# Kernel tuning notes

Measured on AMD Instinct MI355X. Metric: run time of the kernel, lower is better.

Reference implementation:

```python
import jax, jax.numpy as jnp
import numpy as np

B, S, D, H = 4, 2048, 1024, 16
DH = D // H


def setup_inputs() -> dict:
    key = jax.random.key(0)
    ks = jax.random.split(key, 7)
    return {
        "Q": jax.random.normal(ks[0], (B, S, D), dtype=jnp.float32),
        "K": jax.random.normal(ks[1], (B, S, D), dtype=jnp.float32),
        "V": jax.random.normal(ks[2], (B, S, D), dtype=jnp.float32),
        "q_proj": jax.random.normal(ks[3], (D, D), dtype=jnp.float32),
        "k_proj": jax.random.normal(ks[4], (D, D), dtype=jnp.float32),
        "v_proj": jax.random.normal(ks[5], (D, D), dtype=jnp.float32),
        "output_proj": jax.random.normal(ks[6], (D, D), dtype=jnp.float32),
        "casual": 1,
    }


def reference(Q, K, V, q_proj, k_proj, v_proj, output_proj, casual):
    # projections: einsum('... a b, ... s b -> ... s a') == x @ W.T
    q = jnp.einsum('bsd,ad->bsa', Q, q_proj)
    k = jnp.einsum('bsd,ad->bsa', K, k_proj)
    v = jnp.einsum('bsd,ad->bsa', V, v_proj)
    # split heads: [B, S, H, DH]
    q = q.reshape(B, S, H, DH)
    k = k.reshape(B, S, H, DH)
    v = v.reshape(B, S, H, DH)
    # scores [B, H, Sq, Sk]
    scores = jnp.einsum('bqhd,bkhd->bhqk', q, k) / np.sqrt(DH).astype(np.float32)
    # causal mask: 0 on lower triangle, -inf above
    causal_mask = jnp.where(
        jnp.tril(jnp.ones((S, S), dtype=bool)), 0.0, -jnp.inf
    ).astype(scores.dtype)
    scores = scores + causal_mask
    attn = jax.nn.softmax(scores, axis=-1)
    # weighted values -> [B, Sq, H, DH] -> [B, Sq, D]
    out = jnp.einsum('bhqk,bkhd->bqhd', attn, v).reshape(B, S, D)
    # output projection: einsum('... a b, ... b -> ... a') == x @ W.T
    return jnp.einsum('bsd,ad->bsa', out, output_proj)
```

## Files before the change

### kernel.cpp

```cpp
#include <hip/hip_runtime.h>


typedef __attribute__((ext_vector_type(8))) _Float16 half8;
typedef __attribute__((ext_vector_type(4))) float f32x4;

#define DEVI static __device__ __forceinline__

static constexpr int cB = 4, cS = 2048, cD = 1024, cH = 16, cDH = 64;
static constexpr int cM = cB * cS;

DEVI unsigned short h2b(_Float16 h) { union { _Float16 f; unsigned short u; } x; x.f = h; return x.u; }

DEVI void async16(const void* g, void* l) {
#if defined(__HIP_DEVICE_COMPILE__)
  __builtin_amdgcn_global_load_lds((const __attribute__((address_space(1))) unsigned int*)g,
                                   (__attribute__((address_space(3))) unsigned int*)l, 16, 0, 0);
#endif
}

__global__ void split4_kernel(const float* __restrict__ Wq, const float* __restrict__ Wk,
                              const float* __restrict__ Wv, const float* __restrict__ Wo,
                              unsigned short* __restrict__ Wqh, unsigned short* __restrict__ Wql,
                              unsigned short* __restrict__ Wkh, unsigned short* __restrict__ Wkl,
                              unsigned short* __restrict__ Wvh, unsigned short* __restrict__ Woh) {
  const int w = blockIdx.x >> 10, blk = blockIdx.x & 1023;
  const float* in = (w == 0) ? Wq : (w == 1) ? Wk : (w == 2) ? Wv : Wo;
  unsigned short* hi = (w == 0) ? Wqh : (w == 1) ? Wkh : (w == 2) ? Wvh : Woh;
  unsigned short* lo = (w == 0) ? Wql : (w == 1) ? Wkl : nullptr;
  int i = (blk * 256 + (int)threadIdx.x) * 4;
  float4 v = *(const float4*)(in + i);
  _Float16 h0 = (_Float16)v.x, h1 = (_Float16)v.y, h2 = (_Float16)v.z, h3 = (_Float16)v.w;
  unsigned short th[4] = {h2b(h0), h2b(h1), h2b(h2), h2b(h3)};
  *(uint2*)(hi + i) = *(const uint2*)th;
  if (lo != nullptr) {
    unsigned short tl[4] = {h2b((_Float16)(v.x - (float)h0)), h2b((_Float16)(v.y - (float)h1)),
                            h2b((_Float16)(v.z - (float)h2)), h2b((_Float16)(v.w - (float)h3))};
    *(uint2*)(lo + i) = *(const uint2*)tl;
  }
}

__global__ void split_act_kernel(const float* __restrict__ Q, const float* __restrict__ K,
                                 unsigned short* __restrict__ Qh, unsigned short* __restrict__ Ql,
                                 unsigned short* __restrict__ Kh, unsigned short* __restrict__ Kl) {
  const int t = blockIdx.x >> 13;
  const int blk = blockIdx.x & 8191;
  const float* in = t ? K : Q;
  unsigned short* hi = t ? Kh : Qh;
  unsigned short* lo = t ? Kl : Ql;
  int i = (blk * 256 + (int)threadIdx.x) * 4;
  float4 v = *(const float4*)(in + i);
  _Float16 h0 = (_Float16)v.x, h1 = (_Float16)v.y, h2 = (_Float16)v.z, h3 = (_Float16)v.w;
  unsigned short th[4] = {h2b(h0), h2b(h1), h2b(h2), h2b(h3)};
  *(uint2*)(hi + i) = *(const uint2*)th;
  unsigned short tl[4] = {h2b((_Float16)(v.x - (float)h0)), h2b((_Float16)(v.y - (float)h1)),
                          h2b((_Float16)(v.z - (float)h2)), h2b((_Float16)(v.w - (float)h3))};
  *(uint2*)(lo + i) = *(const uint2*)tl;
}

__global__ __launch_bounds__(256, 2) void proj_qk(
    const unsigned short* __restrict__ Qh, const unsigned short* __restrict__ Ql,
    const unsigned short* __restrict__ Kh, const unsigned short* __restrict__ Kl,
    const unsigned short* __restrict__ Wqh, const unsigned short* __restrict__ Wql,
    const unsigned short* __restrict__ Wkh, const unsigned short* __restrict__ Wkl,
    unsigned short* __restrict__ qph, unsigned short* __restrict__ qpl,
    unsigned short* __restrict__ kph, unsigned short* __restrict__ kpl) {
  constexpr int N = cD, K = cD;
  __shared__ unsigned short sAh[2][128 * 32];
  __shared__ unsigned short sAl[2][128 * 32];
  __shared__ unsigned short sBh[2][128 * 32];
  __shared__ unsigned short sBl[2][128 * 32];

  const int wid = ((int)blockIdx.x & 7) * 128 + ((int)blockIdx.x >> 3);
  const int job = wid >> 9;
  const int bid = wid & 511;
  const unsigned short* Ah_g = job ? Kh : Qh;
  const unsigned short* Al_g = job ? Kl : Ql;
  const unsigned short* Bh = job ? Wkh : Wqh;
  const unsigned short* Bl = job ? Wkl : Wql;
  unsigned short* C0 = job ? kph : qph;
  unsigned short* C1 = job ? kpl : qpl;

  const int tid = threadIdx.x, lane = tid & 63, wave = tid >> 6;
  const int wm = wave >> 1, wn = wave & 1;
  const int bm = bid >> 3, bn = bid & 7;
  const long r0 = (long)bm * 128, c0 = (long)bn * 128;
  const int quad = lane >> 4, cl = lane & 15;
  const int lrow16 = lane >> 2, lg4 = lane & 3;

  f32x4 acc[4][4];
#pragma unroll
  for (int mt = 0; mt < 4; ++mt)
#pragma unroll
    for (int nt = 0; nt < 4; ++nt) acc[mt][nt] = f32x4{0.f, 0.f, 0.f, 0.f};

  auto stage = [&](int k0, int buf) {
#pragma unroll
    for (int c = 0; c < 2; ++c) {
      int cc = wave * 2 + c;
      int r = cc * 16 + lrow16;
      int sw = (lg4 ^ ((lrow16 >> 1) & 3)) * 8;
      long ga = (r0 + r) * (long)K + k0 + sw;
      long gb = (c0 + r) * (long)K + k0 + sw;
      async16(Ah_g + ga, &sAh[buf][cc * 512]);
      async16(Al_g + ga, &sAl[buf][cc * 512]);
      async16(Bh + gb, &sBh[buf][cc * 512]);
      async16(Bl + gb, &sBl[buf][cc * 512]);
    }
  };

  auto compute = [&](int buf) {
    half8 ah[4], al[4], bh8[4], bl8[4];
#pragma unroll
    for (int mt = 0; mt < 4; ++mt) {
      int r = wm * 64 + mt * 16 + cl;
      int s = quad ^ ((r >> 1) & 3);
      ah[mt] = *(const half8*)(&sAh[buf][r * 32 + s * 8]);
      al[mt] = *(const half8*)(&sAl[buf][r * 32 + s * 8]);
    }
#pragma unroll
    for (int nt = 0; nt < 4; ++nt) {
      int r = wn * 64 + nt * 16 + cl;
      int s = quad ^ ((r >> 1) & 3);
      bh8[nt] = *(const half8*)(&sBh[buf][r * 32 + s * 8]);
      bl8[nt] = *(const half8*)(&sBl[buf][r * 32 + s * 8]);
    }
#pragma unroll
    for (int mt = 0; mt < 4; ++mt)
#pragma unroll
      for (int nt = 0; nt < 4; ++nt) {
        acc[mt][nt] = __builtin_amdgcn_mfma_f32_16x16x32_f16(ah[mt], bh8[nt], acc[mt][nt], 0, 0, 0);
        acc[mt][nt] = __builtin_amdgcn_mfma_f32_16x16x32_f16(ah[mt], bl8[nt], acc[mt][nt], 0, 0, 0);
        acc[mt][nt] = __builtin_amdgcn_mfma_f32_16x16x32_f16(al[mt], bh8[nt], acc[mt][nt], 0, 0, 0);
      }
  };

  stage(0, 0);
  __syncthreads();
  int cur = 0;
  for (int k0 = 32; k0 < K; k0 += 32) {
    stage(k0, cur ^ 1);
    compute(cur);
    __syncthreads();
    cur ^= 1;
  }
  compute(cur);

#pragma unroll
  for (int mt = 0; mt < 4; ++mt)
#pragma unroll
    for (int nt = 0; nt < 4; ++nt)
#pragma unroll
      for (int i = 0; i < 4; ++i) {
        long row = r0 + wm * 64 + mt * 16 + quad * 4 + i;
        long col = c0 + wn * 64 + nt * 16 + cl;
        float v = acc[mt][nt][i];
        _Float16 hh = (_Float16)v;
        C0[row * N + col] = h2b(hh);
        C1[row * N + col] = h2b((_Float16)(v - (float)hh));
      }
}

__global__ __launch_bounds__(256, 3) void proj_v(const float* __restrict__ Va,
                                                 const unsigned short* __restrict__ Wvh,
                                                 unsigned short* __restrict__ vp) {
  constexpr int N = cD, K = cD;
  __shared__ float sA32[2][128 * 32];
  __shared__ unsigned short sBh[2][128 * 32];

  const int wid = ((int)blockIdx.x & 7) * 64 + ((int)blockIdx.x >> 3);
  const int bm = wid >> 3, bn = wid & 7;
  const long r0 = (long)bm * 128, c0 = (long)bn * 128;

  const int tid = threadIdx.x, lane = tid & 63, wave = tid >> 6;
  const int wm = wave >> 1, wn = wave & 1;
  const int quad = lane >> 4, cl = lane & 15;
  const int lrow8 = lane >> 3, lg8 = lane & 7;
  const int lrow16 = lane >> 2, lg4 = lane & 3;

  f32x4 acc[4][4];
#pragma unroll
  for (int mt = 0; mt < 4; ++mt)
#pragma unroll
    for (int nt = 0; nt < 4; ++nt) acc[mt][nt] = f32x4{0.f, 0.f, 0.f, 0.f};

  auto stage = [&](int k0, int buf) {
#pragma unroll
    for (int c = 0; c < 4; ++c) {
      int cc = wave * 4 + c;
      int r = cc * 8 + lrow8;
      const float* g = Va + (r0 + r) * (long)K + k0 + ((lg8 ^ lrow8) * 4);
      async16(g, &sA32[buf][cc * 256]);
    }
#pragma unroll
    for (int c = 0; c < 2; ++c) {
      int cc = wave * 2 + c;
      int r = cc * 16 + lrow16;
      long gb = (c0 + r) * (long)K + k0 + ((lg4 ^ ((lrow16 >> 1) & 3)) * 8);
      async16(Wvh + gb, &sBh[buf][cc * 512]);
    }
  };

  auto compute = [&](int buf) {
    half8 ah[4], bh8[4];
#pragma unroll
    for (int mt = 0; mt < 4; ++mt) {
      int r = wm * 64 + mt * 16 + cl;
      int s0 = (quad * 2 + 0) ^ (r & 7), s1 = (quad * 2 + 1) ^ (r & 7);
      float fa[8];
      *(float4*)(fa) = *(const float4*)(&sA32[buf][r * 32 + s0 * 4]);
      *(float4*)(fa + 4) = *(const float4*)(&sA32[buf][r * 32 + s1 * 4]);
#pragma unroll
      for (int j = 0; j < 8; ++j) ah[mt][j] = (_Float16)fa[j];
    }
#pragma unroll
    for (int nt = 0; nt < 4; ++nt) {
      int r = wn * 64 + nt * 16 + cl;
      int s = quad ^ ((r >> 1) & 3);
      bh8[nt] = *(const half8*)(&sBh[buf][r * 32 + s * 8]);
    }
#pragma unroll
    for (int mt = 0; mt < 4; ++mt)
#pragma unroll
      for (int nt = 0; nt < 4; ++nt)
        acc[mt][nt] = __builtin_amdgcn_mfma_f32_16x16x32_f16(ah[mt], bh8[nt], acc[mt][nt], 0, 0, 0);
  };

  stage(0, 0);
  __syncthreads();
  int cur = 0;
  for (int k0 = 32; k0 < K; k0 += 32) {
    stage(k0, cur ^ 1);
    compute(cur);
    __syncthreads();
    cur ^= 1;
  }
  compute(cur);

#pragma unroll
  for (int mt = 0; mt < 4; ++mt)
#pragma unroll
    for (int nt = 0; nt < 4; ++nt)
#pragma unroll
      for (int i = 0; i < 4; ++i) {
        long row = r0 + wm * 64 + mt * 16 + quad * 4 + i;
        long col = c0 + wn * 64 + nt * 16 + cl;
        vp[row * N + col] = h2b((_Float16)acc[mt][nt][i]);
      }
}

__global__ __launch_bounds__(256, 3) void gemm_out(const unsigned short* __restrict__ A16p,
                                                   const unsigned short* __restrict__ Bh,
                                                   float* __restrict__ C0, int M, int N, int K) {
  __shared__ unsigned short sA16[2][128 * 32];
  __shared__ unsigned short sB16[2][128 * 32];

  const int tid = threadIdx.x, lane = tid & 63, wave = tid >> 6;
  const int wm = wave >> 1, wn = wave & 1;
  const int nb = N >> 7;
  const int wid = ((int)blockIdx.x & 7) * 64 + ((int)blockIdx.x >> 3);
  const int bm = wid / nb, bn = wid % nb;
  const long r0 = (long)bm * 128, c0 = (long)bn * 128;
  const int quad = lane >> 4, cl = lane & 15;
  const int lrow16 = lane >> 2, lg4 = lane & 3;

  f32x4 acc[4][4];
#pragma unroll
  for (int mt = 0; mt < 4; ++mt)
#pragma unroll
    for (int nt = 0; nt < 4; ++nt) acc[mt][nt] = f32x4{0.f, 0.f, 0.f, 0.f};

  auto stage = [&](int k0, int buf) {
#pragma unroll
    for (int c = 0; c < 2; ++c) {
      int cc = wave * 2 + c;
      int r = cc * 16 + lrow16;
      int sw = (lg4 ^ ((lrow16 >> 1) & 3)) * 8;
      async16(A16p + (r0 + r) * (long)K + k0 + sw, &sA16[buf][cc * 512]);
      async16(Bh + (c0 + r) * (long)K + k0 + sw, &sB16[buf][cc * 512]);
    }
  };

  auto compute = [&](int buf) {
    half8 ah[4], bh8[4];
#pragma unroll
    for (int mt = 0; mt < 4; ++mt) {
      int r = wm * 64 + mt * 16 + cl;
      int s = quad ^ ((r >> 1) & 3);
      ah[mt] = *(const half8*)(&sA16[buf][r * 32 + s * 8]);
    }
#pragma unroll
    for (int nt = 0; nt < 4; ++nt) {
      int r = wn * 64 + nt * 16 + cl;
      int s = quad ^ ((r >> 1) & 3);
      bh8[nt] = *(const half8*)(&sB16[buf][r * 32 + s * 8]);
    }
#pragma unroll
    for (int mt = 0; mt < 4; ++mt)
#pragma unroll
      for (int nt = 0; nt < 4; ++nt)
        acc[mt][nt] = __builtin_amdgcn_mfma_f32_16x16x32_f16(ah[mt], bh8[nt], acc[mt][nt], 0, 0, 0);
  };

  stage(0, 0);
  __syncthreads();
  int cur = 0;
  for (int k0 = 32; k0 < K; k0 += 32) {
    stage(k0, cur ^ 1);
    compute(cur);
    __syncthreads();
    cur ^= 1;
  }
  compute(cur);

#pragma unroll
  for (int mt = 0; mt < 4; ++mt)
#pragma unroll
    for (int nt = 0; nt < 4; ++nt)
#pragma unroll
      for (int i = 0; i < 4; ++i) {
        long row = r0 + wm * 64 + mt * 16 + quad * 4 + i;
        long col = c0 + wn * 64 + nt * 16 + cl;
        C0[row * N + col] = acc[mt][nt][i];
      }
}

__global__ __launch_bounds__(256, 3) void flash_kernel(
    const unsigned short* __restrict__ qh_g, const unsigned short* __restrict__ ql_g,
    const unsigned short* __restrict__ kh_g, const unsigned short* __restrict__ kl_g,
    const unsigned short* __restrict__ vp_g, unsigned short* __restrict__ out) {
  __shared__ unsigned short sKh[64 * 64];
  __shared__ unsigned short sKl[64 * 64];
  __shared__ unsigned int sVtU[64 * 34];
  __shared__ unsigned short sP[4][32 * 40];

  const int tid = threadIdx.x, lane = tid & 63, wave = tid >> 6;
  const int quad = lane >> 4, cl = lane & 15;
  const int bh = blockIdx.x & 63;
  const int qt = 15 - (blockIdx.x >> 6);
  const int h = bh & 15;
  const int b = bh >> 4;
  const long rowbase = (long)b * cS;
  const int q0 = qt * 128;
  const int lrow8 = lane >> 3, lg8 = lane & 7;

  half8 qh[2][2], ql[2][2];
  const _Float16 s8 = (_Float16)0.125f;
#pragma unroll
  for (int ks = 0; ks < 2; ++ks)
#pragma unroll
    for (int mt = 0; mt < 2; ++mt) {
      long r = rowbase + q0 + wave * 32 + mt * 16 + cl;
      long off = r * cD + h * 64 + ks * 32 + quad * 8;
      qh[ks][mt] = *(const half8*)(qh_g + off) * s8;
      ql[ks][mt] = *(const half8*)(ql_g + off) * s8;
    }

  f32x4 O[2][5];
  float mrow[2][4];
#pragma unroll
  for (int mt = 0; mt < 2; ++mt) {
#pragma unroll
    for (int dt = 0; dt < 5; ++dt) O[mt][dt] = f32x4{0.f, 0.f, 0.f, 0.f};
#pragma unroll
    for (int i = 0; i < 4; ++i) mrow[mt][i] = -1e30f;
  }

  half8 vone;
#pragma unroll
  for (int j = 0; j < 8; ++j) vone[j] = (cl == 0) ? (_Float16)1.0f : (_Float16)0.0f;

  auto tile = [&](int ki, bool MASK) {
    __syncthreads();
#pragma unroll
    for (int c = 0; c < 2; ++c) {
      int cc = wave * 2 + c;
      int r = cc * 8 + lrow8;
      long g = (rowbase + ki * 64 + r) * (long)cD + h * 64 + ((lg8 ^ lrow8) * 8);
      async16(kh_g + g, sKh + cc * 512);
      async16(kl_g + g, sKl + cc * 512);
    }
    {
      int r2 = tid & 31, dc = (tid >> 5) * 8;
      const unsigned short* gv = vp_g + (rowbase + ki * 64 + 2 * r2) * (long)cD + h * 64 + dc;
      unsigned short a[8], bb[8];
      *(uint4*)a = *(const uint4*)gv;
      *(uint4*)bb = *(const uint4*)(gv + cD);
#pragma unroll
      for (int j = 0; j < 8; ++j)
        sVtU[(dc + j) * 34 + r2] = (unsigned int)a[j] | ((unsigned int)bb[j] << 16);
    }
    __syncthreads();

    f32x4 sacc[2][4];
#pragma unroll
    for (int mt = 0; mt < 2; ++mt)
#pragma unroll
      for (int nt = 0; nt < 4; ++nt) sacc[mt][nt] = f32x4{0.f, 0.f, 0.f, 0.f};
#pragma unroll
    for (int ks = 0; ks < 2; ++ks) {
      half8 kh8[4], kl8[4];
#pragma unroll
      for (int nt = 0; nt < 4; ++nt) {
        int r = nt * 16 + cl;
        int off = r * 64 + (((ks * 4 + quad) ^ (r & 7)) * 8);
        kh8[nt] = *(const half8*)(sKh + off);
        kl8[nt] = *(const half8*)(sKl + off);
      }
#pragma unroll
      for (int mt = 0; mt < 2; ++mt)
#pragma unroll
        for (int nt = 0; nt < 4; ++nt) {
          sacc[mt][nt] = __builtin_amdgcn_mfma_f32_16x16x32_f16(qh[ks][mt], kh8[nt], sacc[mt][nt], 0, 0, 0);
          sacc[mt][nt] = __builtin_amdgcn_mfma_f32_16x16x32_f16(qh[ks][mt], kl8[nt], sacc[mt][nt], 0, 0, 0);
          sacc[mt][nt] = __builtin_amdgcn_mfma_f32_16x16x32_f16(ql[ks][mt], kh8[nt], sacc[mt][nt], 0, 0, 0);
        }
    }
    if (MASK) {
#pragma unroll
      for (int mt = 0; mt < 2; ++mt)
#pragma unroll
        for (int nt = 0; nt < 4; ++nt)
#pragma unroll
          for (int i = 0; i < 4; ++i) {
            int rg = q0 + wave * 32 + mt * 16 + quad * 4 + i;
            int cg = ki * 64 + nt * 16 + cl;
            if (cg > rg) sacc[mt][nt][i] = -1e30f;
          }
    }
    float mnew[2][4];
    bool ch = false;
#pragma unroll
    for (int mt = 0; mt < 2; ++mt)
#pragma unroll
      for (int i = 0; i < 4; ++i) {
        float mx = fmaxf(fmaxf(sacc[mt][0][i], sacc[mt][1][i]),
                         fmaxf(sacc[mt][2][i], sacc[mt][3][i]));
#pragma unroll
        for (int d = 1; d < 16; d <<= 1) mx = fmaxf(mx, __shfl_xor(mx, d));
        ch |= (mx > mrow[mt][i]);
        mnew[mt][i] = fmaxf(mrow[mt][i], mx);
      }
    if (__ballot(ch)) {
#pragma unroll
      for (int mt = 0; mt < 2; ++mt)
#pragma unroll
        for (int i = 0; i < 4; ++i) {
          float a = __expf(mrow[mt][i] - mnew[mt][i]);
#pragma unroll
          for (int dt = 0; dt < 5; ++dt) O[mt][dt][i] *= a;
        }
    }
#pragma unroll
    for (int mt = 0; mt < 2; ++mt)
#pragma unroll
      for (int i = 0; i < 4; ++i) mrow[mt][i] = mnew[mt][i];

    unsigned short* sPw = sP[wave];
#pragma unroll
    for (int kc = 0; kc < 2; ++kc) {
#pragma unroll
      for (int mt = 0; mt < 2; ++mt)
#pragma unroll
        for (int ntl = 0; ntl < 2; ++ntl) {
          int nt = kc * 2 + ntl;
#pragma unroll
          for (int i = 0; i < 4; ++i) {
            float p = __expf(sacc[mt][nt][i] - mrow[mt][i]);
            sPw[(mt * 16 + quad * 4 + i) * 40 + ntl * 16 + cl] = h2b((_Float16)p);
          }
        }
      half8 pa[2], vb[4];
#pragma unroll
      for (int mt = 0; mt < 2; ++mt)
        pa[mt] = *(const half8*)(sPw + (mt * 16 + cl) * 40 + quad * 8);
#pragma unroll
      for (int dt = 0; dt < 4; ++dt) {
        int base = (dt * 16 + cl) * 34 + kc * 16 + quad * 4;
        union { uint4 u; half8 hh; } cvt;
        uint2 p0 = *(const uint2*)(sVtU + base);
        uint2 p1 = *(const uint2*)(sVtU + base + 2);
        cvt.u = uint4{p0.x, p0.y, p1.x, p1.y};
        vb[dt] = cvt.hh;
      }
#pragma unroll
      for (int mt = 0; mt < 2; ++mt) {
#pragma unroll
        for (int dt = 0; dt < 4; ++dt)
          O[mt][dt] = __builtin_amdgcn_mfma_f32_16x16x32_f16(pa[mt], vb[dt], O[mt][dt], 0, 0, 0);
        O[mt][4] = __builtin_amdgcn_mfma_f32_16x16x32_f16(pa[mt], vone, O[mt][4], 0, 0, 0);
      }
    }
  };

  const int full = 2 * qt;
  for (int ki = 0; ki < full; ++ki) tile(ki, false);
  tile(full, true);
  tile(full + 1, true);

  float lv[2][4];
#pragma unroll
  for (int mt = 0; mt < 2; ++mt)
#pragma unroll
    for (int i = 0; i < 4; ++i) lv[mt][i] = __shfl(O[mt][4][i], (lane & 48));
#pragma unroll
  for (int mt = 0; mt < 2; ++mt)
#pragma unroll
    for (int dt = 0; dt < 4; ++dt)
#pragma unroll
      for (int i = 0; i < 4; ++i) {
        long r = rowbase + q0 + wave * 32 + mt * 16 + quad * 4 + i;
        out[r * cD + h * 64 + dt * 16 + cl] = h2b((_Float16)(O[mt][dt][i] / lv[mt][i]));
      }
}

extern "C" void kernel_launch(void* const* d_in, const int* in_sizes, int n_in,
                              void* d_out, int out_size, void* d_ws, size_t ws_size,
                              hipStream_t stream) {
  const float* Q = (const float*)d_in[0];
  const float* K = (const float*)d_in[1];
  const float* V = (const float*)d_in[2];
  const float* Wq = (const float*)d_in[3];
  const float* Wk = (const float*)d_in[4];
  const float* Wv = (const float*)d_in[5];
  const float* Wo = (const float*)d_in[6];

  unsigned short* ws = (unsigned short*)d_ws;
  const size_t WD = (size_t)cD * cD;
  const size_t WM = (size_t)cM * cD;
  unsigned short* Wqh = ws;
  unsigned short* Wql = Wqh + WD;
  unsigned short* Wkh = Wql + WD;
  unsigned short* Wkl = Wkh + WD;
  unsigned short* Wvh = Wkl + WD;
  unsigned short* Woh = Wvh + WD;
  unsigned short* R1 = Woh + WD;
  unsigned short* R2 = R1 + WM;
  unsigned short* qph = R2 + WM;
  unsigned short* qpl = qph + WM;
  unsigned short* kph = qpl + WM;
  unsigned short* kpl = kph + WM;

  unsigned short* Qh = (unsigned short*)d_out;
  unsigned short* Ql = Qh + WM;
  unsigned short* Kh = R1;
  unsigned short* Kl = R2;
  unsigned short* vp = R1;
  unsigned short* attnb = R2;

  split4_kernel<<<4096, 256, 0, stream>>>(Wq, Wk, Wv, Wo, Wqh, Wql, Wkh, Wkl, Wvh, Woh);
  split_act_kernel<<<16384, 256, 0, stream>>>(Q, K, Qh, Ql, Kh, Kl);

  proj_qk<<<1024, 256, 0, stream>>>(Qh, Ql, Kh, Kl, Wqh, Wql, Wkh, Wkl,
                                    qph, qpl, kph, kpl);
  proj_v<<<512, 256, 0, stream>>>(V, Wvh, vp);

  flash_kernel<<<cB * cH * 16, 256, 0, stream>>>(qph, qpl, kph, kpl, vp, attnb);

  const int gblk = (cM / 128) * (cD / 128);
  gemm_out<<<gblk, 256, 0, stream>>>(attnb, Woh, (float*)d_out, cM, cD, cD);
}
```

Before: 509.1 us.

## Fuse activation hi/lo split into QK projection and raise MFMA priority in flash

Drops the separate activation split kernel. proj_qk now loads fp32 Q/K tiles straight into LDS with an XOR swizzle and splits them into fp16 hi/lo inside the compute loop. This removes a full write and re-read of the split activations in global memory, at the cost of extra conversion ALU work in the GEMM inner loop and twice the LDS footprint for the A tile. It also wraps the flash-attention MFMA blocks in s_setprio to favour matrix issue, and reassigns the workspace buffers.

```diff
diff --git a/kernel.cpp b/kernel.cpp
--- a/kernel.cpp
+++ b/kernel.cpp
@@ -39,42 +39,21 @@
   }
 }
 
-__global__ void split_act_kernel(const float* __restrict__ Q, const float* __restrict__ K,
-                                 unsigned short* __restrict__ Qh, unsigned short* __restrict__ Ql,
-                                 unsigned short* __restrict__ Kh, unsigned short* __restrict__ Kl) {
-  const int t = blockIdx.x >> 13;
-  const int blk = blockIdx.x & 8191;
-  const float* in = t ? K : Q;
-  unsigned short* hi = t ? Kh : Qh;
-  unsigned short* lo = t ? Kl : Ql;
-  int i = (blk * 256 + (int)threadIdx.x) * 4;
-  float4 v = *(const float4*)(in + i);
-  _Float16 h0 = (_Float16)v.x, h1 = (_Float16)v.y, h2 = (_Float16)v.z, h3 = (_Float16)v.w;
-  unsigned short th[4] = {h2b(h0), h2b(h1), h2b(h2), h2b(h3)};
-  *(uint2*)(hi + i) = *(const uint2*)th;
-  unsigned short tl[4] = {h2b((_Float16)(v.x - (float)h0)), h2b((_Float16)(v.y - (float)h1)),
-                          h2b((_Float16)(v.z - (float)h2)), h2b((_Float16)(v.w - (float)h3))};
-  *(uint2*)(lo + i) = *(const uint2*)tl;
-}
-
 __global__ __launch_bounds__(256, 2) void proj_qk(
-    const unsigned short* __restrict__ Qh, const unsigned short* __restrict__ Ql,
-    const unsigned short* __restrict__ Kh, const unsigned short* __restrict__ Kl,
+    const float* __restrict__ Qa, const float* __restrict__ Ka,
     const unsigned short* __restrict__ Wqh, const unsigned short* __restrict__ Wql,
     const unsigned short* __restrict__ Wkh, const unsigned short* __restrict__ Wkl,
     unsigned short* __restrict__ qph, unsigned short* __restrict__ qpl,
     unsigned short* __restrict__ kph, unsigned short* __restrict__ kpl) {
   constexpr int N = cD, K = cD;
-  __shared__ unsigned short sAh[2][128 * 32];
-  __shared__ unsigned short sAl[2][128 * 32];
+  __shared__ float sA32[2][128 * 32];
   __shared__ unsigned short sBh[2][128 * 32];
   __shared__ unsigned short sBl[2][128 * 32];
 
   const int wid = ((int)blockIdx.x & 7) * 128 + ((int)blockIdx.x >> 3);
   const int job = wid >> 9;
   const int bid = wid & 511;
-  const unsigned short* Ah_g = job ? Kh : Qh;
-  const unsigned short* Al_g = job ? Kl : Ql;
+  const float* A32p = job ? Ka : Qa;
   const unsigned short* Bh = job ? Wkh : Wqh;
   const unsigned short* Bl = job ? Wkl : Wql;
   unsigned short* C0 = job ? kph : qph;
@@ -85,6 +64,7 @@
   const int bm = bid >> 3, bn = bid & 7;
   const long r0 = (long)bm * 128, c0 = (long)bn * 128;
   const int quad = lane >> 4, cl = lane & 15;
+  const int lrow8 = lane >> 3, lg8 = lane & 7;
   const int lrow16 = lane >> 2, lg4 = lane & 3;
 
   f32x4 acc[4][4];
@@ -94,15 +74,18 @@
     for (int nt = 0; nt < 4; ++nt) acc[mt][nt] = f32x4{0.f, 0.f, 0.f, 0.f};
 
   auto stage = [&](int k0, int buf) {
+#pragma unroll
+    for (int c = 0; c < 4; ++c) {
+      int cc = wave * 4 + c;
+      int r = cc * 8 + lrow8;
+      const float* g = A32p + (r0 + r) * (long)K + k0 + ((lg8 ^ lrow8) * 4);
+      async16(g, &sA32[buf][cc * 256]);
+    }
 #pragma unroll
     for (int c = 0; c < 2; ++c) {
       int cc = wave * 2 + c;
       int r = cc * 16 + lrow16;
-      int sw = (lg4 ^ ((lrow16 >> 1) & 3)) * 8;
-      long ga = (r0 + r) * (long)K + k0 + sw;
-      long gb = (c0 + r) * (long)K + k0 + sw;
-      async16(Ah_g + ga, &sAh[buf][cc * 512]);
-      async16(Al_g + ga, &sAl[buf][cc * 512]);
+      long gb = (c0 + r) * (long)K + k0 + ((lg4 ^ ((lrow16 >> 1) & 3)) * 8);
       async16(Bh + gb, &sBh[buf][cc * 512]);
       async16(Bl + gb, &sBl[buf][cc * 512]);
     }
@@ -113,9 +96,16 @@
 #pragma unroll
     for (int mt = 0; mt < 4; ++mt) {
       int r = wm * 64 + mt * 16 + cl;
-      int s = quad ^ ((r >> 1) & 3);
-      ah[mt] = *(const half8*)(&sAh[buf][r * 32 + s * 8]);
-      al[mt] = *(const half8*)(&sAl[buf][r * 32 + s * 8]);
+      int s0 = (quad * 2 + 0) ^ (r & 7), s1 = (quad * 2 + 1) ^ (r & 7);
+      float fa[8];
+      *(float4*)(fa) = *(const float4*)(&sA32[buf][r * 32 + s0 * 4]);
+      *(float4*)(fa + 4) = *(const float4*)(&sA32[buf][r * 32 + s1 * 4]);
+#pragma unroll
+      for (int j = 0; j < 8; ++j) {
+        _Float16 hh = (_Float16)fa[j];
+        ah[mt][j] = hh;
+        al[mt][j] = (_Float16)(fa[j] - (float)hh);
+      }
     }
 #pragma unroll
     for (int nt = 0; nt < 4; ++nt) {
@@ -406,6 +396,7 @@
         kh8[nt] = *(const half8*)(sKh + off);
         kl8[nt] = *(const half8*)(sKl + off);
       }
+      __builtin_amdgcn_s_setprio(1);
 #pragma unroll
       for (int mt = 0; mt < 2; ++mt)
 #pragma unroll
@@ -414,6 +405,7 @@
           sacc[mt][nt] = __builtin_amdgcn_mfma_f32_16x16x32_f16(qh[ks][mt], kl8[nt], sacc[mt][nt], 0, 0, 0);
           sacc[mt][nt] = __builtin_amdgcn_mfma_f32_16x16x32_f16(ql[ks][mt], kh8[nt], sacc[mt][nt], 0, 0, 0);
         }
+      __builtin_amdgcn_s_setprio(0);
     }
     if (MASK) {
 #pragma unroll
@@ -482,6 +474,7 @@
         cvt.u = uint4{p0.x, p0.y, p1.x, p1.y};
         vb[dt] = cvt.hh;
       }
+      __builtin_amdgcn_s_setprio(1);
 #pragma unroll
       for (int mt = 0; mt < 2; ++mt) {
 #pragma unroll
@@ -489,6 +482,7 @@
           O[mt][dt] = __builtin_amdgcn_mfma_f32_16x16x32_f16(pa[mt], vb[dt], O[mt][dt], 0, 0, 0);
         O[mt][4] = __builtin_amdgcn_mfma_f32_16x16x32_f16(pa[mt], vone, O[mt][4], 0, 0, 0);
       }
+      __builtin_amdgcn_s_setprio(0);
     }
   };
 
@@ -533,25 +527,16 @@
   unsigned short* Wkl = Wkh + WD;
   unsigned short* Wvh = Wkl + WD;
   unsigned short* Woh = Wvh + WD;
-  unsigned short* R1 = Woh + WD;
-  unsigned short* R2 = R1 + WM;
-  unsigned short* qph = R2 + WM;
+  unsigned short* qph = Woh + WD;
   unsigned short* qpl = qph + WM;
   unsigned short* kph = qpl + WM;
   unsigned short* kpl = kph + WM;
-
-  unsigned short* Qh = (unsigned short*)d_out;
-  unsigned short* Ql = Qh + WM;
-  unsigned short* Kh = R1;
-  unsigned short* Kl = R2;
-  unsigned short* vp = R1;
-  unsigned short* attnb = R2;
+  unsigned short* vp = kpl + WM;
+  unsigned short* attnb = vp + WM;
 
   split4_kernel<<<4096, 256, 0, stream>>>(Wq, Wk, Wv, Wo, Wqh, Wql, Wkh, Wkl, Wvh, Woh);
-  split_act_kernel<<<16384, 256, 0, stream>>>(Q, K, Qh, Ql, Kh, Kl);
-
-  proj_qk<<<1024, 256, 0, stream>>>(Qh, Ql, Kh, Kl, Wqh, Wql, Wkh, Wkl,
-                                    qph, qpl, kph, kpl);
+
+  proj_qk<<<1024, 256, 0, stream>>>(Q, K, Wqh, Wql, Wkh, Wkl, qph, qpl, kph, kpl);
   proj_v<<<512, 256, 0, stream>>>(V, Wvh, vp);
 
   flash_kernel<<<cB * cH * 16, 256, 0, stream>>>(qph, qpl, kph, kpl, vp, attnb);
```

Measured after the change: 537.0 us. 1.05x slower.

## Replace double-buffered LDS pipelines in projection GEMMs with single-buffer sync loops

Applied to the files above, without the earlier changes.

The proj_qk, proj_v and gemm_out kernels drop their double-buffered shared-memory prefetch and become a simple loop: sync, issue async global-to-LDS loads, sync, compute. This halves LDS use per block, which could allow more resident blocks. The launch-bounds occupancy hints also change (proj_qk raised to 3 blocks, gemm_out lowered to 2). The cost is that global loads no longer overlap MFMA compute within a block, so latency hiding now depends on other resident blocks.

```diff
diff --git a/kernel.cpp b/kernel.cpp
--- a/kernel.cpp
+++ b/kernel.cpp
@@ -57,7 +57,7 @@
   *(uint2*)(lo + i) = *(const uint2*)tl;
 }
 
-__global__ __launch_bounds__(256, 2) void proj_qk(
+__global__ __launch_bounds__(256, 3) void proj_qk(
     const unsigned short* __restrict__ Qh, const unsigned short* __restrict__ Ql,
     const unsigned short* __restrict__ Kh, const unsigned short* __restrict__ Kl,
     const unsigned short* __restrict__ Wqh, const unsigned short* __restrict__ Wql,
@@ -65,10 +65,10 @@
     unsigned short* __restrict__ qph, unsigned short* __restrict__ qpl,
     unsigned short* __restrict__ kph, unsigned short* __restrict__ kpl) {
   constexpr int N = cD, K = cD;
-  __shared__ unsigned short sAh[2][128 * 32];
-  __shared__ unsigned short sAl[2][128 * 32];
-  __shared__ unsigned short sBh[2][128 * 32];
-  __shared__ unsigned short sBl[2][128 * 32];
+  __shared__ unsigned short sAh[128 * 32];
+  __shared__ unsigned short sAl[128 * 32];
+  __shared__ unsigned short sBh[128 * 32];
+  __shared__ unsigned short sBl[128 * 32];
 
   const int wid = ((int)blockIdx.x & 7) * 128 + ((int)blockIdx.x >> 3);
   const int job = wid >> 9;
@@ -93,7 +93,8 @@
 #pragma unroll
     for (int nt = 0; nt < 4; ++nt) acc[mt][nt] = f32x4{0.f, 0.f, 0.f, 0.f};
 
-  auto stage = [&](int k0, int buf) {
+  for (int k0 = 0; k0 < K; k0 += 32) {
+    __syncthreads();
 #pragma unroll
     for (int c = 0; c < 2; ++c) {
       int cc = wave * 2 + c;
@@ -101,28 +102,27 @@
       int sw = (lg4 ^ ((lrow16 >> 1) & 3)) * 8;
       long ga = (r0 + r) * (long)K + k0 + sw;
       long gb = (c0 + r) * (long)K + k0 + sw;
-      async16(Ah_g + ga, &sAh[buf][cc * 512]);
-      async16(Al_g + ga, &sAl[buf][cc * 512]);
-      async16(Bh + gb, &sBh[buf][cc * 512]);
-      async16(Bl + gb, &sBl[buf][cc * 512]);
-    }
-  };
-
-  auto compute = [&](int buf) {
+      async16(Ah_g + ga, sAh + cc * 512);
+      async16(Al_g + ga, sAl + cc * 512);
+      async16(Bh + gb, sBh + cc * 512);
+      async16(Bl + gb, sBl + cc * 512);
+    }
+    __syncthreads();
+
     half8 ah[4], al[4], bh8[4], bl8[4];
 #pragma unroll
     for (int mt = 0; mt < 4; ++mt) {
       int r = wm * 64 + mt * 16 + cl;
       int s = quad ^ ((r >> 1) & 3);
-      ah[mt] = *(const half8*)(&sAh[buf][r * 32 + s * 8]);
-      al[mt] = *(const half8*)(&sAl[buf][r * 32 + s * 8]);
+      ah[mt] = *(const half8*)(sAh + r * 32 + s * 8);
+      al[mt] = *(const half8*)(sAl + r * 32 + s * 8);
     }
 #pragma unroll
     for (int nt = 0; nt < 4; ++nt) {
       int r = wn * 64 + nt * 16 + cl;
       int s = quad ^ ((r >> 1) & 3);
-      bh8[nt] = *(const half8*)(&sBh[buf][r * 32 + s * 8]);
-      bl8[nt] = *(const half8*)(&sBl[buf][r * 32 + s * 8]);
+      bh8[nt] = *(const half8*)(sBh + r * 32 + s * 8);
+      bl8[nt] = *(const half8*)(sBl + r * 32 + s * 8);
     }
 #pragma unroll
     for (int mt = 0; mt < 4; ++mt)
@@ -132,18 +132,7 @@
         acc[mt][nt] = __builtin_amdgcn_mfma_f32_16x16x32_f16(ah[mt], bl8[nt], acc[mt][nt], 0, 0, 0);
         acc[mt][nt] = __builtin_amdgcn_mfma_f32_16x16x32_f16(al[mt], bh8[nt], acc[mt][nt], 0, 0, 0);
       }
-  };
-
-  stage(0, 0);
-  __syncthreads();
-  int cur = 0;
-  for (int k0 = 32; k0 < K; k0 += 32) {
-    stage(k0, cur ^ 1);
-    compute(cur);
-    __syncthreads();
-    cur ^= 1;
   }
-  compute(cur);
 
 #pragma unroll
   for (int mt = 0; mt < 4; ++mt)
@@ -164,8 +153,8 @@
                                                  const unsigned short* __restrict__ Wvh,
                                                  unsigned short* __restrict__ vp) {
   constexpr int N = cD, K = cD;
-  __shared__ float sA32[2][128 * 32];
-  __shared__ unsigned short sBh[2][128 * 32];
+  __shared__ float sA32[128 * 32];
+  __shared__ unsigned short sBh[128 * 32];
 
   const int wid = ((int)blockIdx.x & 7) * 64 + ((int)blockIdx.x >> 3);
   const int bm = wid >> 3, bn = wid & 7;
@@ -183,32 +172,32 @@
 #pragma unroll
     for (int nt = 0; nt < 4; ++nt) acc[mt][nt] = f32x4{0.f, 0.f, 0.f, 0.f};
 
-  auto stage = [&](int k0, int buf) {
+  for (int k0 = 0; k0 < K; k0 += 32) {
+    __syncthreads();
 #pragma unroll
     for (int c = 0; c < 4; ++c) {
       int cc = wave * 4 + c;
       int r = cc * 8 + lrow8;
       const float* g = Va + (r0 + r) * (long)K + k0 + ((lg8 ^ lrow8) * 4);
-      async16(g, &sA32[buf][cc * 256]);
+      async16(g, sA32 + cc * 256);
     }
 #pragma unroll
     for (int c = 0; c < 2; ++c) {
       int cc = wave * 2 + c;
       int r = cc * 16 + lrow16;
       long gb = (c0 + r) * (long)K + k0 + ((lg4 ^ ((lrow16 >> 1) & 3)) * 8);
-      async16(Wvh + gb, &sBh[buf][cc * 512]);
-    }
-  };
-
-  auto compute = [&](int buf) {
+      async16(Wvh + gb, sBh + cc * 512);
+    }
+    __syncthreads();
+
     half8 ah[4], bh8[4];
 #pragma unroll
     for (int mt = 0; mt < 4; ++mt) {
       int r = wm * 64 + mt * 16 + cl;
       int s0 = (quad * 2 + 0) ^ (r & 7), s1 = (quad * 2 + 1) ^ (r & 7);
       float fa[8];
-      *(float4*)(fa) = *(const float4*)(&sA32[buf][r * 32 + s0 * 4]);
-      *(float4*)(fa + 4) = *(const float4*)(&sA32[buf][r * 32 + s1 * 4]);
+      *(float4*)(fa) = *(const float4*)(sA32 + r * 32 + s0 * 4);
+      *(float4*)(fa + 4) = *(const float4*)(sA32 + r * 32 + s1 * 4);
 #pragma unroll
       for (int j = 0; j < 8; ++j) ah[mt][j] = (_Float16)fa[j];
     }
@@ -216,25 +205,14 @@
     for (int nt = 0; nt < 4; ++nt) {
       int r = wn * 64 + nt * 16 + cl;
       int s = quad ^ ((r >> 1) & 3);
-      bh8[nt] = *(const half8*)(&sBh[buf][r * 32 + s * 8]);
+      bh8[nt] = *(const half8*)(sBh + r * 32 + s * 8);
     }
 #pragma unroll
     for (int mt = 0; mt < 4; ++mt)
 #pragma unroll
       for (int nt = 0; nt < 4; ++nt)
         acc[mt][nt] = __builtin_amdgcn_mfma_f32_16x16x32_f16(ah[mt], bh8[nt], acc[mt][nt], 0, 0, 0);
-  };
-
-  stage(0, 0);
-  __syncthreads();
-  int cur = 0;
-  for (int k0 = 32; k0 < K; k0 += 32) {
-    stage(k0, cur ^ 1);
-    compute(cur);
-    __syncthreads();
-    cur ^= 1;
   }
-  compute(cur);
 
 #pragma unroll
   for (int mt = 0; mt < 4; ++mt)
@@ -248,11 +226,11 @@
       }
 }
 
-__global__ __launch_bounds__(256, 3) void gemm_out(const unsigned short* __restrict__ A16p,
+__global__ __launch_bounds__(256, 2) void gemm_out(const unsigned short* __restrict__ A16p,
                                                    const unsigned short* __restrict__ Bh,
                                                    float* __restrict__ C0, int M, int N, int K) {
-  __shared__ unsigned short sA16[2][128 * 32];
-  __shared__ unsigned short sB16[2][128 * 32];
+  __shared__ unsigned short sA16[128 * 32];
+  __shared__ unsigned short sB16[128 * 32];
 
   const int tid = threadIdx.x, lane = tid & 63, wave = tid >> 6;
   const int wm = wave >> 1, wn = wave & 1;
@@ -269,48 +247,37 @@
 #pragma unroll
     for (int nt = 0; nt < 4; ++nt) acc[mt][nt] = f32x4{0.f, 0.f, 0.f, 0.f};
 
-  auto stage = [&](int k0, int buf) {
+  for (int k0 = 0; k0 < K; k0 += 32) {
+    __syncthreads();
 #pragma unroll
     for (int c = 0; c < 2; ++c) {
       int cc = wave * 2 + c;
       int r = cc * 16 + lrow16;
       int sw = (lg4 ^ ((lrow16 >> 1) & 3)) * 8;
-      async16(A16p + (r0 + r) * (long)K + k0 + sw, &sA16[buf][cc * 512]);
-      async16(Bh + (c0 + r) * (long)K + k0 + sw, &sB16[buf][cc * 512]);
-    }
-  };
-
-  auto compute = [&](int buf) {
+      async16(A16p + (r0 + r) * (long)K + k0 + sw, sA16 + cc * 512);
+      async16(Bh + (c0 + r) * (long)K + k0 + sw, sB16 + cc * 512);
+    }
+    __syncthreads();
+
     half8 ah[4], bh8[4];
 #pragma unroll
     for (int mt = 0; mt < 4; ++mt) {
       int r = wm * 64 + mt * 16 + cl;
       int s = quad ^ ((r >> 1) & 3);
-      ah[mt] = *(const half8*)(&sA16[buf][r * 32 + s * 8]);
+      ah[mt] = *(const half8*)(sA16 + r * 32 + s * 8);
     }
 #pragma unroll
     for (int nt = 0; nt < 4; ++nt) {
       int r = wn * 64 + nt * 16 + cl;
       int s = quad ^ ((r >> 1) & 3);
-      bh8[nt] = *(const half8*)(&sB16[buf][r * 32 + s * 8]);
+      bh8[nt] = *(const half8*)(sB16 + r * 32 + s * 8);
     }
 #pragma unroll
     for (int mt = 0; mt < 4; ++mt)
 #pragma unroll
       for (int nt = 0; nt < 4; ++nt)
         acc[mt][nt] = __builtin_amdgcn_mfma_f32_16x16x32_f16(ah[mt], bh8[nt], acc[mt][nt], 0, 0, 0);
-  };
-
-  stage(0, 0);
-  __syncthreads();
-  int cur = 0;
-  for (int k0 = 32; k0 < K; k0 += 32) {
-    stage(k0, cur ^ 1);
-    compute(cur);
-    __syncthreads();
-    cur ^= 1;
   }
-  compute(cur);
 
 #pragma unroll
   for (int mt = 0; mt < 4; ++mt)
```

Measured after the change: 487.6 us. 4.2% less time.
